# Kernel optimization log

Measured on AMD Instinct MI355X. Metric: run time of the kernel, lower is better.

## Reference

```python
import jax, jax.numpy as jnp
import numpy as np

B, IN, OUT = 128, 1024, 1024


def setup_inputs() -> dict:
    key = jax.random.key(0)
    ks = jax.random.split(key, 7)
    return {
        "x": jax.random.normal(ks[0], (B, IN), dtype=jnp.float32),
        "weight_mu": jax.random.normal(ks[1], (OUT, IN), dtype=jnp.float32) * 0.05,
        "weight_rho": jax.random.normal(ks[2], (OUT, IN), dtype=jnp.float32) - 5.0,
        "bias_mu": jax.random.normal(ks[3], (OUT,), dtype=jnp.float32) * 0.05,
        "bias_rho": jax.random.normal(ks[4], (OUT,), dtype=jnp.float32) - 5.0,
        "eps_w": jax.random.normal(ks[5], (B, OUT, IN), dtype=jnp.float32),
        "eps_b": jax.random.normal(ks[6], (B, OUT), dtype=jnp.float32),
    }


def reference(x, weight_mu, weight_rho, bias_mu, bias_rho, eps_w, eps_b):
    # Reparameterized per-sample weights: w_b = mu + softplus(rho) * eps_b  -> (B, OUT, IN)
    weight = weight_mu[None, :, :] + jax.nn.softplus(weight_rho)[None, :, :] * eps_w
    # Batched matvec: x[:,None,:] @ w_b^T  ==  einsum over the input dim
    out = jnp.einsum("bi,boi->bo", x, weight)
    # Per-sample bias: (B, OUT)
    bias = bias_mu[None, :] + jax.nn.softplus(bias_rho)[None, :] * eps_b
    return out + bias
```

## Files before the change

### kernel.cpp

```cpp
#include <hip/hip_runtime.h>
#include <math.h>

#define BATCH 128
#define DIN   1024
#define DOUT  1024
#define NO    16

__device__ __forceinline__ float softplus_f(float v) {
    return fmaxf(v, 0.0f) + log1pf(__expf(-fabsf(v)));
}

__device__ __forceinline__ unsigned bf16_rne(float f) {
    unsigned u = __float_as_uint(f);
    return (u + 0x7FFFu + ((u >> 16) & 1u)) >> 16;
}

__global__ __launch_bounds__(256) void pack_qm_kernel(
    const float* __restrict__ wmu,
    const float* __restrict__ wrho,
    const float* __restrict__ brho,
    unsigned* __restrict__ qm,
    float* __restrict__ bsp)
{
    const int idx = blockIdx.x * 256 + threadIdx.x;
    const float4 m4 = reinterpret_cast<const float4*>(wmu)[idx];
    const float4 r4 = reinterpret_cast<const float4*>(wrho)[idx];
    uint4 w;
    w.x = (bf16_rne(softplus_f(r4.x)) << 16) | bf16_rne(m4.x);
    w.y = (bf16_rne(softplus_f(r4.y)) << 16) | bf16_rne(m4.y);
    w.z = (bf16_rne(softplus_f(r4.z)) << 16) | bf16_rne(m4.z);
    w.w = (bf16_rne(softplus_f(r4.w)) << 16) | bf16_rne(m4.w);
    reinterpret_cast<uint4*>(qm)[idx] = w;

    if (blockIdx.x < 4) {
        const int o = blockIdx.x * 256 + threadIdx.x;
        bsp[o] = softplus_f(brho[o]);
    }
}

__global__ __launch_bounds__(256) void bayes_main_kernel(
    const float* __restrict__ x,
    const unsigned* __restrict__ qm,
    const float* __restrict__ bmu,
    const float* __restrict__ bsp,
    const float* __restrict__ epsw,
    const float* __restrict__ epsb,
    float* __restrict__ out)
{
    const int wid  = blockIdx.x * 4 + (threadIdx.x >> 6);
    const int lane = threadIdx.x & 63;
    const int b  = wid >> 6;
    const int o0 = (wid & 63) * NO;

    const float4* __restrict__ x4 = reinterpret_cast<const float4*>(x + (size_t)b * DIN);
    float xv[16];
    #pragma unroll
    for (int k = 0; k < 4; ++k) {
        const float4 t = x4[lane + (k << 6)];
        xv[4*k+0] = t.x; xv[4*k+1] = t.y; xv[4*k+2] = t.z; xv[4*k+3] = t.w;
    }

    const float4* __restrict__ e4base =
        reinterpret_cast<const float4*>(epsw + ((size_t)b * DOUT + o0) * DIN);
    const uint4* __restrict__ q4base =
        reinterpret_cast<const uint4*>(qm + (size_t)o0 * DIN);

    float acc[NO];

    #pragma unroll
    for (int oo = 0; oo < NO; ++oo) {
        const float4* __restrict__ e4 = e4base + (size_t)oo * (DIN / 4);
        const uint4*  __restrict__ q4 = q4base + (size_t)oo * (DIN / 4);
        float a = 0.0f;
        #pragma unroll
        for (int k = 0; k < 4; ++k) {
            const int idx = lane + (k << 6);
            const float4 ee = e4[idx];
            const uint4  ww = q4[idx];
            const float mu0 = __uint_as_float(ww.x << 16);
            const float q0  = __uint_as_float(ww.x & 0xffff0000u);
            const float mu1 = __uint_as_float(ww.y << 16);
            const float q1  = __uint_as_float(ww.y & 0xffff0000u);
            const float mu2 = __uint_as_float(ww.z << 16);
            const float q2  = __uint_as_float(ww.z & 0xffff0000u);
            const float mu3 = __uint_as_float(ww.w << 16);
            const float q3  = __uint_as_float(ww.w & 0xffff0000u);
            a = fmaf(xv[4*k+0], fmaf(q0, ee.x, mu0), a);
            a = fmaf(xv[4*k+1], fmaf(q1, ee.y, mu1), a);
            a = fmaf(xv[4*k+2], fmaf(q2, ee.z, mu2), a);
            a = fmaf(xv[4*k+3], fmaf(q3, ee.w, mu3), a);
        }
        acc[oo] = a;
    }

    #pragma unroll
    for (int oo = 0; oo < NO; ++oo) {
        #pragma unroll
        for (int off = 32; off >= 1; off >>= 1)
            acc[oo] += __shfl_xor(acc[oo], off, 64);
    }

    if (lane == 0) {
        #pragma unroll
        for (int oo = 0; oo < NO; ++oo) {
            const int o = o0 + oo;
            const size_t row = (size_t)b * DOUT + o;
            out[row] = acc[oo] + fmaf(bsp[o], epsb[row], bmu[o]);
        }
    }
}

extern "C" void kernel_launch(void* const* d_in, const int* in_sizes, int n_in,
                              void* d_out, int out_size, void* d_ws, size_t ws_size,
                              hipStream_t stream) {
    const float* x    = (const float*)d_in[0];
    const float* wmu  = (const float*)d_in[1];
    const float* wrho = (const float*)d_in[2];
    const float* bmu  = (const float*)d_in[3];
    const float* brho = (const float*)d_in[4];
    const float* epsw = (const float*)d_in[5];
    const float* epsb = (const float*)d_in[6];
    float* out = (float*)d_out;

    unsigned* qm  = (unsigned*)d_ws;
    float*    bsp = (float*)((char*)d_ws + (size_t)DOUT * DIN * sizeof(unsigned));

    pack_qm_kernel<<<(DOUT * DIN / 4) / 256, 256, 0, stream>>>(wmu, wrho, brho, qm, bsp);

    bayes_main_kernel<<<8192 / 4, 256, 0, stream>>>(x, qm, bmu, bsp, epsw, epsb, out);
}
```

Baseline: 120.7 us.

## Stage eps and packed weights through LDS with async double-buffered loads

Replaces direct global vector loads in the main kernel with per-wave double-buffered staging into shared memory via global_load_lds. Explicit vmcnt and lgkmcnt waits and scheduling barriers are meant to keep the next row's loads in flight while the current row is computed. This aims to hide memory latency in the bandwidth-bound matvec. It costs 64 KB of LDS per block, which may reduce occupancy, and adds an extra LDS read pass.

```diff
diff --git a/kernel.cpp b/kernel.cpp
--- a/kernel.cpp
+++ b/kernel.cpp
@@ -1,10 +1,12 @@
 #include <hip/hip_runtime.h>
 #include <math.h>
+#include <stdint.h>
 
 #define BATCH 128
 #define DIN   1024
 #define DOUT  1024
 #define NO    16
+#define DEPTH 2
 
 __device__ __forceinline__ float softplus_f(float v) {
     return fmaxf(v, 0.0f) + log1pf(__expf(-fabsf(v)));
@@ -13,6 +15,13 @@
 __device__ __forceinline__ unsigned bf16_rne(float f) {
     unsigned u = __float_as_uint(f);
     return (u + 0x7FFFu + ((u >> 16) & 1u)) >> 16;
+}
+
+__device__ __forceinline__ void stage16(const void* gsrc, void* ldst) {
+    __builtin_amdgcn_global_load_lds(
+        (const __attribute__((address_space(1))) uint32_t*)gsrc,
+        (__attribute__((address_space(3))) uint32_t*)ldst,
+        16, 0, 0);
 }
 
 __global__ __launch_bounds__(256) void pack_qm_kernel(
@@ -47,8 +56,10 @@
     const float* __restrict__ epsb,
     float* __restrict__ out)
 {
-    const int wid  = blockIdx.x * 4 + (threadIdx.x >> 6);
+    __shared__ __align__(16) uint8_t smem[4][DEPTH][8192];
+    const int w    = threadIdx.x >> 6;
     const int lane = threadIdx.x & 63;
+    const int wid  = blockIdx.x * 4 + w;
     const int b  = wid >> 6;
     const int o0 = (wid & 63) * NO;
 
@@ -60,52 +71,73 @@
         xv[4*k+0] = t.x; xv[4*k+1] = t.y; xv[4*k+2] = t.z; xv[4*k+3] = t.w;
     }
 
-    const float4* __restrict__ e4base =
-        reinterpret_cast<const float4*>(epsw + ((size_t)b * DOUT + o0) * DIN);
-    const uint4* __restrict__ q4base =
-        reinterpret_cast<const uint4*>(qm + (size_t)o0 * DIN);
+    const float*    erow = epsw + ((size_t)b * DOUT + o0) * DIN;
+    const unsigned* qrow = qm + (size_t)o0 * DIN;
+
+    auto stage_row = [&](int r, int s) {
+        const float*    eg = erow + (size_t)r * DIN + lane * 4;
+        const unsigned* qg = qrow + (size_t)r * DIN + lane * 4;
+        uint8_t* le = &smem[w][s][0];
+        uint8_t* lq = &smem[w][s][4096];
+        #pragma unroll
+        for (int t = 0; t < 4; ++t) {
+            stage16(eg + t * 256, le + t * 1024);
+            stage16(qg + t * 256, lq + t * 1024);
+        }
+    };
+
+    stage_row(0, 0);
+    stage_row(1, 1);
 
     float acc[NO];
 
     #pragma unroll
-    for (int oo = 0; oo < NO; ++oo) {
-        const float4* __restrict__ e4 = e4base + (size_t)oo * (DIN / 4);
-        const uint4*  __restrict__ q4 = q4base + (size_t)oo * (DIN / 4);
+    for (int r = 0; r < NO; ++r) {
+        const int s = r & 1;
+        if (r < NO - 1) asm volatile("s_waitcnt vmcnt(8)" ::: "memory");
+        else            asm volatile("s_waitcnt vmcnt(0)" ::: "memory");
+        __builtin_amdgcn_sched_barrier(0);
+
+        const float4* __restrict__ eL = reinterpret_cast<const float4*>(&smem[w][s][0]);
+        const uint4*  __restrict__ qL = reinterpret_cast<const uint4*>(&smem[w][s][4096]);
+        float4 ee[4]; uint4 ww[4];
+        #pragma unroll
+        for (int k = 0; k < 4; ++k) {
+            ee[k] = eL[lane + (k << 6)];
+            ww[k] = qL[lane + (k << 6)];
+        }
+        asm volatile("s_waitcnt lgkmcnt(0)" ::: "memory");
+        __builtin_amdgcn_sched_barrier(0);
+        if (r + DEPTH < NO) stage_row(r + DEPTH, s);
+
         float a = 0.0f;
         #pragma unroll
         for (int k = 0; k < 4; ++k) {
-            const int idx = lane + (k << 6);
-            const float4 ee = e4[idx];
-            const uint4  ww = q4[idx];
-            const float mu0 = __uint_as_float(ww.x << 16);
-            const float q0  = __uint_as_float(ww.x & 0xffff0000u);
-            const float mu1 = __uint_as_float(ww.y << 16);
-            const float q1  = __uint_as_float(ww.y & 0xffff0000u);
-            const float mu2 = __uint_as_float(ww.z << 16);
-            const float q2  = __uint_as_float(ww.z & 0xffff0000u);
-            const float mu3 = __uint_as_float(ww.w << 16);
-            const float q3  = __uint_as_float(ww.w & 0xffff0000u);
-            a = fmaf(xv[4*k+0], fmaf(q0, ee.x, mu0), a);
-            a = fmaf(xv[4*k+1], fmaf(q1, ee.y, mu1), a);
-            a = fmaf(xv[4*k+2], fmaf(q2, ee.z, mu2), a);
-            a = fmaf(xv[4*k+3], fmaf(q3, ee.w, mu3), a);
+            a = fmaf(xv[4*k+0], fmaf(__uint_as_float(ww[k].x & 0xffff0000u), ee[k].x,
+                                     __uint_as_float(ww[k].x << 16)), a);
+            a = fmaf(xv[4*k+1], fmaf(__uint_as_float(ww[k].y & 0xffff0000u), ee[k].y,
+                                     __uint_as_float(ww[k].y << 16)), a);
+            a = fmaf(xv[4*k+2], fmaf(__uint_as_float(ww[k].z & 0xffff0000u), ee[k].z,
+                                     __uint_as_float(ww[k].z << 16)), a);
+            a = fmaf(xv[4*k+3], fmaf(__uint_as_float(ww[k].w & 0xffff0000u), ee[k].w,
+                                     __uint_as_float(ww[k].w << 16)), a);
         }
-        acc[oo] = a;
+        acc[r] = a;
     }
 
     #pragma unroll
-    for (int oo = 0; oo < NO; ++oo) {
+    for (int r = 0; r < NO; ++r) {
         #pragma unroll
         for (int off = 32; off >= 1; off >>= 1)
-            acc[oo] += __shfl_xor(acc[oo], off, 64);
+            acc[r] += __shfl_xor(acc[r], off, 64);
     }
 
     if (lane == 0) {
+        const size_t row0 = (size_t)b * DOUT + o0;
         #pragma unroll
-        for (int oo = 0; oo < NO; ++oo) {
-            const int o = o0 + oo;
-            const size_t row = (size_t)b * DOUT + o;
-            out[row] = acc[oo] + fmaf(bsp[o], epsb[row], bmu[o]);
+        for (int r = 0; r < NO; ++r) {
+            const int o = o0 + r;
+            out[row0 + r] = acc[r] + fmaf(bsp[o], epsb[row0 + r], bmu[o]);
         }
     }
 }
```

Measured after the change: 130.4 us. 1.08x slower.
